# Performance work log

Hardware: AMD Instinct MI355X
Metric: run time of the kernel (lower is better)

Reference implementation:

```python
import jax, jax.numpy as jnp
import numpy as np

CODE_DISTANCE = 3
ERROR_THRESHOLD = 1e-06
CORRECTION_STRENGTH = 0.1


def setup_inputs() -> dict:
    key = jax.random.key(0)
    k1, k2, k3, k4, k5 = jax.random.split(key, 5)
    d = CODE_DISTANCE
    params = jax.random.normal(k1, (2048, 12288), dtype=jnp.float32)
    # nn.Linear-style init scale (uniform-ish magnitude); exact dist irrelevant for correctness harness
    W_syn = jax.random.normal(k2, (d, d), dtype=jnp.float32) * (1.0 / np.sqrt(d))
    b_syn = jax.random.normal(k3, (d,), dtype=jnp.float32) * (1.0 / np.sqrt(d))
    W_corr = jax.random.normal(k4, (3, d, d), dtype=jnp.float32) * (1.0 / np.sqrt(d))
    b_corr = jax.random.normal(k5, (3, d), dtype=jnp.float32) * (1.0 / np.sqrt(d))
    return {"params": params, "W_syn": W_syn, "b_syn": b_syn,
            "W_corr": W_corr, "b_corr": b_corr}


def reference(params, W_syn, b_syn, W_corr, b_corr):
    d = CODE_DISTANCE
    orig_shape = params.shape
    n = params.size
    flat = params.reshape(-1)
    pad = (-n) % d  # static; 0 for our chosen shape
    if pad:
        flat = jnp.pad(flat, (0, pad))
    blocks = flat.reshape(-1, d)                      # [N, d]

    # syndrome detection: Linear(d, d) -> x @ W^T + b
    syndromes = blocks @ W_syn.T + b_syn              # [N, d]
    error_mag = jnp.linalg.norm(syndromes, axis=1)    # [N]
    error_mask = error_mag > ERROR_THRESHOLD          # [N]

    # correction_j(block) = block @ W_corr[j]^T + b_corr[j]; j ranges over 3 ops (= d)
    # corr_out: [3, N, d]
    corr_out = jnp.einsum('nd,jkd->jnk', blocks, W_corr) + b_corr[:, None, :]
    # correction_i = sum_j syndromes[i, j] * corr_out[j, i, :]
    correction = jnp.einsum('nj,jnd->nd', syndromes, corr_out)  # [N, d]

    corrected = jnp.where(error_mask[:, None],
                          blocks - CORRECTION_STRENGTH * correction,
                          blocks)
    out = corrected.reshape(-1)[:n].reshape(orig_shape)
    return out
```

## Files before the change

### kernel.cpp

```cpp
#include <hip/hip_runtime.h>
#include <hip/hip_bf16.h>

#define CORR_STRENGTH 0.1f
#define ERR_THRESH2 1e-12f

typedef float floatx4 __attribute__((ext_vector_type(4)));

__global__ void __launch_bounds__(256) qec_kernel(
    const float* __restrict__ params,
    const float* __restrict__ Wsyn,
    const float* __restrict__ bsyn,
    const float* __restrict__ Wcorr,
    const float* __restrict__ bcorr,
    float* __restrict__ out,
    long long nvec,
    long long nblk)
{
    float ws[9], bs[3], wc[27], bc[9];
#pragma unroll
    for (int i = 0; i < 9; ++i)  ws[i] = Wsyn[i];
#pragma unroll
    for (int i = 0; i < 3; ++i)  bs[i] = bsyn[i];
#pragma unroll
    for (int i = 0; i < 27; ++i) wc[i] = Wcorr[i];
#pragma unroll
    for (int i = 0; i < 9; ++i)  bc[i] = bcorr[i];

    const long long tid     = (long long)blockIdx.x * blockDim.x + threadIdx.x;
    const long long nthread = (long long)gridDim.x * blockDim.x;

    const floatx4* __restrict__ src4 = reinterpret_cast<const floatx4*>(params);
    floatx4* __restrict__       dst4 = reinterpret_cast<floatx4*>(out);

    for (long long idx = tid; idx < nvec; idx += nthread) {
        floatx4 a = src4[idx * 3 + 0];
        floatx4 b = src4[idx * 3 + 1];
        floatx4 c = src4[idx * 3 + 2];

        float x[12] = { a.x, a.y, a.z, a.w,
                        b.x, b.y, b.z, b.w,
                        c.x, c.y, c.z, c.w };
        float y[12];

#pragma unroll
        for (int bl = 0; bl < 4; ++bl) {
            const float x0 = x[bl * 3 + 0];
            const float x1 = x[bl * 3 + 1];
            const float x2 = x[bl * 3 + 2];

            float s[3];
#pragma unroll
            for (int k = 0; k < 3; ++k)
                s[k] = fmaf(ws[k * 3 + 0], x0,
                        fmaf(ws[k * 3 + 1], x1,
                         fmaf(ws[k * 3 + 2], x2, bs[k])));

            const float mag2 = s[0] * s[0] + s[1] * s[1] + s[2] * s[2];
            const bool active = mag2 > ERR_THRESH2;

            float corr[3] = {0.f, 0.f, 0.f};
#pragma unroll
            for (int j = 0; j < 3; ++j) {
#pragma unroll
                for (int k = 0; k < 3; ++k) {
                    const float co = fmaf(wc[j * 9 + k * 3 + 0], x0,
                                      fmaf(wc[j * 9 + k * 3 + 1], x1,
                                       fmaf(wc[j * 9 + k * 3 + 2], x2, bc[j * 3 + k])));
                    corr[k] = fmaf(s[j], co, corr[k]);
                }
            }

#pragma unroll
            for (int k = 0; k < 3; ++k) {
                const float xv = x[bl * 3 + k];
                y[bl * 3 + k] = active ? (xv - CORR_STRENGTH * corr[k]) : xv;
            }
        }

        floatx4 o0 = { y[0], y[1], y[2],  y[3]  };
        floatx4 o1 = { y[4], y[5], y[6],  y[7]  };
        floatx4 o2 = { y[8], y[9], y[10], y[11] };
        __builtin_nontemporal_store(o0, &dst4[idx * 3 + 0]);
        __builtin_nontemporal_store(o1, &dst4[idx * 3 + 1]);
        __builtin_nontemporal_store(o2, &dst4[idx * 3 + 2]);
    }

    const long long firstTailBlk = nvec * 4;
    for (long long blk = firstTailBlk + tid; blk < nblk; blk += nthread) {
        const float x0 = params[blk * 3 + 0];
        const float x1 = params[blk * 3 + 1];
        const float x2 = params[blk * 3 + 2];

        float s[3];
#pragma unroll
        for (int k = 0; k < 3; ++k)
            s[k] = fmaf(ws[k * 3 + 0], x0,
                    fmaf(ws[k * 3 + 1], x1,
                     fmaf(ws[k * 3 + 2], x2, bs[k])));

        const float mag2 = s[0] * s[0] + s[1] * s[1] + s[2] * s[2];
        const bool active = mag2 > ERR_THRESH2;

        float corr[3] = {0.f, 0.f, 0.f};
#pragma unroll
        for (int j = 0; j < 3; ++j) {
#pragma unroll
            for (int k = 0; k < 3; ++k) {
                const float co = fmaf(wc[j * 9 + k * 3 + 0], x0,
                                  fmaf(wc[j * 9 + k * 3 + 1], x1,
                                   fmaf(wc[j * 9 + k * 3 + 2], x2, bc[j * 3 + k])));
                corr[k] = fmaf(s[j], co, corr[k]);
            }
        }

        out[blk * 3 + 0] = active ? (x0 - CORR_STRENGTH * corr[0]) : x0;
        out[blk * 3 + 1] = active ? (x1 - CORR_STRENGTH * corr[1]) : x1;
        out[blk * 3 + 2] = active ? (x2 - CORR_STRENGTH * corr[2]) : x2;
    }
}

extern "C" void kernel_launch(void* const* d_in, const int* in_sizes, int n_in,
                              void* d_out, int out_size, void* d_ws, size_t ws_size,
                              hipStream_t stream) {
    const float* params = (const float*)d_in[0];
    const float* Wsyn   = (const float*)d_in[1];
    const float* bsyn   = (const float*)d_in[2];
    const float* Wcorr  = (const float*)d_in[3];
    const float* bcorr  = (const float*)d_in[4];
    float* out = (float*)d_out;

    const long long n    = (long long)in_sizes[0];
    const long long nblk = n / 3;
    const long long nvec = n / 12;

    const int block = 256;
    const int grid  = 2048;

    qec_kernel<<<grid, block, 0, stream>>>(params, Wsyn, bsyn, Wcorr, bcorr,
                                           out, nvec, nblk);
}
```

Before: 44.51 us.

## Stage loads and stores through LDS for fully coalesced float4 access

Each wave now loads 192 contiguous float4s with lane-strided (coalesced) global reads, writes them to shared memory, and reads back the three consecutive vectors each thread needs. Results go back through LDS the same way before coalesced global stores. This replaces the stride-3 float4 global accesses, which spread each wave's requests over more memory lines. The cost is LDS traffic, extra barriers, a grid resized to the tile count (up to 16384 blocks), and plain stores where nontemporal ones were used before.

```diff
diff --git a/kernel.cpp b/kernel.cpp
--- a/kernel.cpp
+++ b/kernel.cpp
@@ -6,6 +6,38 @@
 
 typedef float floatx4 __attribute__((ext_vector_type(4)));
 
+__device__ __forceinline__ void qec_block(
+    const float* __restrict__ ws, const float* __restrict__ bs,
+    const float* __restrict__ wc, const float* __restrict__ bc,
+    float x0, float x1, float x2, float* __restrict__ y)
+{
+    float s[3];
+#pragma unroll
+    for (int k = 0; k < 3; ++k)
+        s[k] = fmaf(ws[k * 3 + 0], x0,
+                fmaf(ws[k * 3 + 1], x1,
+                 fmaf(ws[k * 3 + 2], x2, bs[k])));
+
+    const float mag2 = s[0] * s[0] + s[1] * s[1] + s[2] * s[2];
+    const bool active = mag2 > ERR_THRESH2;
+
+    float corr[3] = {0.f, 0.f, 0.f};
+#pragma unroll
+    for (int j = 0; j < 3; ++j) {
+#pragma unroll
+        for (int k = 0; k < 3; ++k) {
+            const float co = fmaf(wc[j * 9 + k * 3 + 0], x0,
+                              fmaf(wc[j * 9 + k * 3 + 1], x1,
+                               fmaf(wc[j * 9 + k * 3 + 2], x2, bc[j * 3 + k])));
+            corr[k] = fmaf(s[j], co, corr[k]);
+        }
+    }
+
+    y[0] = active ? (x0 - CORR_STRENGTH * corr[0]) : x0;
+    y[1] = active ? (x1 - CORR_STRENGTH * corr[1]) : x1;
+    y[2] = active ? (x2 - CORR_STRENGTH * corr[2]) : x2;
+}
+
 __global__ void __launch_bounds__(256) qec_kernel(
     const float* __restrict__ params,
     const float* __restrict__ Wsyn,
@@ -13,9 +45,12 @@
     const float* __restrict__ Wcorr,
     const float* __restrict__ bcorr,
     float* __restrict__ out,
+    long long nBT,
     long long nvec,
     long long nblk)
 {
+    __shared__ floatx4 lds[4][192];
+
     float ws[9], bs[3], wc[27], bc[9];
 #pragma unroll
     for (int i = 0; i < 9; ++i)  ws[i] = Wsyn[i];
@@ -26,96 +61,85 @@
 #pragma unroll
     for (int i = 0; i < 9; ++i)  bc[i] = bcorr[i];
 
-    const long long tid     = (long long)blockIdx.x * blockDim.x + threadIdx.x;
-    const long long nthread = (long long)gridDim.x * blockDim.x;
+    const int wave = threadIdx.x >> 6;
+    const int lane = threadIdx.x & 63;
 
     const floatx4* __restrict__ src4 = reinterpret_cast<const floatx4*>(params);
     floatx4* __restrict__       dst4 = reinterpret_cast<floatx4*>(out);
 
-    for (long long idx = tid; idx < nvec; idx += nthread) {
-        floatx4 a = src4[idx * 3 + 0];
-        floatx4 b = src4[idx * 3 + 1];
-        floatx4 c = src4[idx * 3 + 2];
+    for (long long bt = blockIdx.x; bt < nBT; bt += gridDim.x) {
+        const long long base4 = bt * 768 + (long long)wave * 192;
+
+        floatx4 v0 = src4[base4 +   0 + lane];
+        floatx4 v1 = src4[base4 +  64 + lane];
+        floatx4 v2 = src4[base4 + 128 + lane];
+        lds[wave][  0 + lane] = v0;
+        lds[wave][ 64 + lane] = v1;
+        lds[wave][128 + lane] = v2;
+        __syncthreads();
+
+        floatx4 a = lds[wave][3 * lane + 0];
+        floatx4 b = lds[wave][3 * lane + 1];
+        floatx4 c = lds[wave][3 * lane + 2];
 
         float x[12] = { a.x, a.y, a.z, a.w,
                         b.x, b.y, b.z, b.w,
                         c.x, c.y, c.z, c.w };
         float y[12];
-
 #pragma unroll
-        for (int bl = 0; bl < 4; ++bl) {
-            const float x0 = x[bl * 3 + 0];
-            const float x1 = x[bl * 3 + 1];
-            const float x2 = x[bl * 3 + 2];
-
-            float s[3];
-#pragma unroll
-            for (int k = 0; k < 3; ++k)
-                s[k] = fmaf(ws[k * 3 + 0], x0,
-                        fmaf(ws[k * 3 + 1], x1,
-                         fmaf(ws[k * 3 + 2], x2, bs[k])));
-
-            const float mag2 = s[0] * s[0] + s[1] * s[1] + s[2] * s[2];
-            const bool active = mag2 > ERR_THRESH2;
-
-            float corr[3] = {0.f, 0.f, 0.f};
-#pragma unroll
-            for (int j = 0; j < 3; ++j) {
-#pragma unroll
-                for (int k = 0; k < 3; ++k) {
-                    const float co = fmaf(wc[j * 9 + k * 3 + 0], x0,
-                                      fmaf(wc[j * 9 + k * 3 + 1], x1,
-                                       fmaf(wc[j * 9 + k * 3 + 2], x2, bc[j * 3 + k])));
-                    corr[k] = fmaf(s[j], co, corr[k]);
-                }
-            }
-
-#pragma unroll
-            for (int k = 0; k < 3; ++k) {
-                const float xv = x[bl * 3 + k];
-                y[bl * 3 + k] = active ? (xv - CORR_STRENGTH * corr[k]) : xv;
-            }
-        }
+        for (int bl = 0; bl < 4; ++bl)
+            qec_block(ws, bs, wc, bc,
+                      x[bl * 3 + 0], x[bl * 3 + 1], x[bl * 3 + 2],
+                      &y[bl * 3]);
 
         floatx4 o0 = { y[0], y[1], y[2],  y[3]  };
         floatx4 o1 = { y[4], y[5], y[6],  y[7]  };
         floatx4 o2 = { y[8], y[9], y[10], y[11] };
-        __builtin_nontemporal_store(o0, &dst4[idx * 3 + 0]);
-        __builtin_nontemporal_store(o1, &dst4[idx * 3 + 1]);
-        __builtin_nontemporal_store(o2, &dst4[idx * 3 + 2]);
+        __syncthreads();
+        lds[wave][3 * lane + 0] = o0;
+        lds[wave][3 * lane + 1] = o1;
+        lds[wave][3 * lane + 2] = o2;
+        __syncthreads();
+
+        floatx4 r0 = lds[wave][  0 + lane];
+        floatx4 r1 = lds[wave][ 64 + lane];
+        floatx4 r2 = lds[wave][128 + lane];
+        dst4[base4 +   0 + lane] = r0;
+        dst4[base4 +  64 + lane] = r1;
+        dst4[base4 + 128 + lane] = r2;
+        __syncthreads();
+    }
+
+    const long long tid     = (long long)blockIdx.x * blockDim.x + threadIdx.x;
+    const long long nthread = (long long)gridDim.x * blockDim.x;
+
+    const long long tailIdx0 = nBT * 256;
+    for (long long idx = tailIdx0 + tid; idx < nvec; idx += nthread) {
+        floatx4 a = src4[idx * 3 + 0];
+        floatx4 b = src4[idx * 3 + 1];
+        floatx4 c = src4[idx * 3 + 2];
+        float x[12] = { a.x, a.y, a.z, a.w,
+                        b.x, b.y, b.z, b.w,
+                        c.x, c.y, c.z, c.w };
+        float y[12];
+#pragma unroll
+        for (int bl = 0; bl < 4; ++bl)
+            qec_block(ws, bs, wc, bc,
+                      x[bl * 3 + 0], x[bl * 3 + 1], x[bl * 3 + 2],
+                      &y[bl * 3]);
+        dst4[idx * 3 + 0] = floatx4{ y[0], y[1], y[2],  y[3]  };
+        dst4[idx * 3 + 1] = floatx4{ y[4], y[5], y[6],  y[7]  };
+        dst4[idx * 3 + 2] = floatx4{ y[8], y[9], y[10], y[11] };
     }
 
     const long long firstTailBlk = nvec * 4;
     for (long long blk = firstTailBlk + tid; blk < nblk; blk += nthread) {
-        const float x0 = params[blk * 3 + 0];
-        const float x1 = params[blk * 3 + 1];
-        const float x2 = params[blk * 3 + 2];
-
-        float s[3];
-#pragma unroll
-        for (int k = 0; k < 3; ++k)
-            s[k] = fmaf(ws[k * 3 + 0], x0,
-                    fmaf(ws[k * 3 + 1], x1,
-                     fmaf(ws[k * 3 + 2], x2, bs[k])));
-
-        const float mag2 = s[0] * s[0] + s[1] * s[1] + s[2] * s[2];
-        const bool active = mag2 > ERR_THRESH2;
-
-        float corr[3] = {0.f, 0.f, 0.f};
-#pragma unroll
-        for (int j = 0; j < 3; ++j) {
-#pragma unroll
-            for (int k = 0; k < 3; ++k) {
-                const float co = fmaf(wc[j * 9 + k * 3 + 0], x0,
-                                  fmaf(wc[j * 9 + k * 3 + 1], x1,
-                                   fmaf(wc[j * 9 + k * 3 + 2], x2, bc[j * 3 + k])));
-                corr[k] = fmaf(s[j], co, corr[k]);
-            }
-        }
-
-        out[blk * 3 + 0] = active ? (x0 - CORR_STRENGTH * corr[0]) : x0;
-        out[blk * 3 + 1] = active ? (x1 - CORR_STRENGTH * corr[1]) : x1;
-        out[blk * 3 + 2] = active ? (x2 - CORR_STRENGTH * corr[2]) : x2;
+        float y[3];
+        qec_block(ws, bs, wc, bc,
+                  params[blk * 3 + 0], params[blk * 3 + 1], params[blk * 3 + 2], y);
+        out[blk * 3 + 0] = y[0];
+        out[blk * 3 + 1] = y[1];
+        out[blk * 3 + 2] = y[2];
     }
 }
 
@@ -129,13 +153,17 @@
     const float* bcorr  = (const float*)d_in[4];
     float* out = (float*)d_out;
 
-    const long long n    = (long long)in_sizes[0];
-    const long long nblk = n / 3;
-    const long long nvec = n / 12;
+    const long long n     = (long long)in_sizes[0];
+    const long long nblk  = n / 3;
+    const long long nvec  = n / 12;
+    const long long nf4   = n / 4;
+    const long long nBT   = nf4 / 768;
 
     const int block = 256;
-    const int grid  = 2048;
+    long long grid_ll = nBT > 0 ? nBT : 1;
+    if (grid_ll > 16384) grid_ll = 16384;
+    const int grid = (int)grid_ll;
 
     qec_kernel<<<grid, block, 0, stream>>>(params, Wsyn, bsyn, Wcorr, bcorr,
-                                           out, nvec, nblk);
+                                           out, nBT, nvec, nblk);
 }
```

Result: faster. 38.07 us (median of 2 runs) (-14.5%).
